# Optimization experiments

Measured on AMD Instinct MI355X. Metric: run time of the kernel, lower is better.

## Reference

```python
import jax, jax.numpy as jnp
import numpy as np

B, C, H, W = 4, 64, 64, 128


def setup_inputs() -> dict:
    key = jax.random.key(0)
    ks = jax.random.split(key, 10)
    s = 1.0 / np.sqrt(C)
    return {
        "query": jax.random.normal(ks[0], (B, C, H, W), dtype=jnp.float32),
        "key_": jax.random.normal(ks[1], (B, C, H, W), dtype=jnp.float32),
        "value": jax.random.normal(ks[2], (B, C, H, W), dtype=jnp.float32),
        "Wq": jax.random.normal(ks[3], (C, C), dtype=jnp.float32) * s,
        "bq": jax.random.normal(ks[4], (C,), dtype=jnp.float32) * s,
        "Wk": jax.random.normal(ks[5], (C, C), dtype=jnp.float32) * s,
        "bk": jax.random.normal(ks[6], (C,), dtype=jnp.float32) * s,
        "Wv": jax.random.normal(ks[7], (C, C), dtype=jnp.float32) * s,
        "bv": jax.random.normal(ks[8], (C,), dtype=jnp.float32) * s,
        "gamma": jax.random.normal(ks[9], (), dtype=jnp.float32) * 0.1,
    }


def reference(query, key_, value, Wq, bq, Wk, bk, Wv, bv, gamma):
    b, c, h, w = query.shape
    n = h * w
    fq = query.reshape(b, c, n)
    fk = key_.reshape(b, c, n)
    fv = value.reshape(b, c, n)
    # 1x1 Conv1d == per-position channel matmul: [C_out, C_in] x [B, C_in, N]
    q = jnp.einsum('oc,bcn->bon', Wq, fq) + bq[:, None]
    k = jnp.einsum('oc,bcn->bon', Wk, fk) + bk[:, None]
    v = jnp.einsum('oc,bcn->bon', Wv, fv) + bv[:, None]
    # query permuted to [B, N, C], bmm with key [B, C, N] -> [B, Nq, Nk]; scale by W (last dim of input shape)
    qk = jnp.einsum('bcn,bcm->bnm', q, k) / w
    # non-standard softmax over dim=1 (query-position axis)
    attn = jax.nn.softmax(qk, axis=1)
    # value [B, C, N] @ attn [B, Nq, Nk] -> [B, C, Nk]
    av = jnp.einsum('bcn,bnm->bcm', v, attn)
    out = gamma * av.reshape(b, c, h, w) + v.reshape(b, c, h, w)
    return out
```

## Files before the change

### kernel.cpp

```cpp
#include <hip/hip_runtime.h>

#define NPOS 8192
#define NC 64
#define NB 4
#define NSPLIT 4
#define NCHUNK 2048
#define QSCALE 0.01127105500167846f

typedef __bf16 bf16x8 __attribute__((ext_vector_type(8)));
typedef __bf16 bf16x4 __attribute__((ext_vector_type(4)));
typedef float f32x4 __attribute__((ext_vector_type(4)));

#define EXP2F(x) __builtin_amdgcn_exp2f(x)

static __device__ __forceinline__ unsigned f2bf_u(float x) {
  unsigned u = __float_as_uint(x);
  return (u + 0x7FFFu + ((u >> 16) & 1u)) >> 16;
}
static __device__ __forceinline__ unsigned pack2(float a, float b) {
  return f2bf_u(a) | (f2bf_u(b) << 16);
}

static __device__ __forceinline__ void gload_lds16(const void* gsrc, void* lds_base) {
  __builtin_amdgcn_global_load_lds(
      (const __attribute__((address_space(1))) unsigned int*)gsrc,
      (__attribute__((address_space(3))) unsigned int*)lds_base, 16, 0, 0);
}

__global__ __launch_bounds__(256) void proj_kernel(
    const float* __restrict__ xq, const float* __restrict__ xk, const float* __restrict__ xv,
    const float* __restrict__ Wq, const float* __restrict__ bq,
    const float* __restrict__ Wk, const float* __restrict__ bk,
    const float* __restrict__ Wv, const float* __restrict__ bv,
    unsigned short* __restrict__ qT, unsigned short* __restrict__ kT,
    unsigned short* __restrict__ vb, float* __restrict__ vf)
{
  __shared__ float sW[NC * NC];
  __shared__ float sB[NC];
  const int p = blockIdx.z, b = blockIdx.y;
  const int n0 = blockIdx.x * 128;
  const int tid = threadIdx.x;
  const int wv = tid >> 6, l = tid & 63;

  const float* x    = p == 0 ? xq : (p == 1 ? xk : xv);
  const float* W    = p == 0 ? Wq : (p == 1 ? Wk : Wv);
  const float* bias = p == 0 ? bq : (p == 1 ? bk : bv);

  for (int i = tid; i < NC * NC; i += 256) sW[i] = W[i];
  if (tid < NC) sB[tid] = bias[tid];
  __syncthreads();

  const int nb = n0 + 2 * l;
  const float* xb = x + (size_t)b * NC * NPOS + nb;

  float acc[16][2];
#pragma unroll
  for (int oi = 0; oi < 16; ++oi) {
    float bz = sB[16 * wv + oi];
    acc[oi][0] = bz; acc[oi][1] = bz;
  }
  for (int c = 0; c < NC; ++c) {
    const float2 x2 = *(const float2*)(xb + (size_t)c * NPOS);
#pragma unroll
    for (int oi = 0; oi < 16; ++oi) {
      float wgt = sW[(16 * wv + oi) * NC + c];
      acc[oi][0] = fmaf(wgt, x2.x, acc[oi][0]);
      acc[oi][1] = fmaf(wgt, x2.y, acc[oi][1]);
    }
  }

  if (p < 2) {
    const float qs = (p == 0) ? QSCALE : 1.0f;
    unsigned short* dst = (p == 0 ? qT : kT) + (size_t)b * NPOS * NC;
#pragma unroll
    for (int r = 0; r < 2; ++r) {
      uint4 w0, w1;
      w0.x = pack2(qs * acc[0][r],  qs * acc[1][r]);
      w0.y = pack2(qs * acc[2][r],  qs * acc[3][r]);
      w0.z = pack2(qs * acc[4][r],  qs * acc[5][r]);
      w0.w = pack2(qs * acc[6][r],  qs * acc[7][r]);
      w1.x = pack2(qs * acc[8][r],  qs * acc[9][r]);
      w1.y = pack2(qs * acc[10][r], qs * acc[11][r]);
      w1.z = pack2(qs * acc[12][r], qs * acc[13][r]);
      w1.w = pack2(qs * acc[14][r], qs * acc[15][r]);
      unsigned short* rp = dst + (size_t)(nb + r) * NC + 16 * wv;
      *(uint4*)(rp) = w0;
      *(uint4*)(rp + 8) = w1;
    }
  } else {
#pragma unroll
    for (int oi = 0; oi < 16; ++oi) {
      const int o = 16 * wv + oi;
      float2 v2;
      v2.x = acc[oi][0]; v2.y = acc[oi][1];
      *(float2*)(vf + ((size_t)b * NC + o) * NPOS + nb) = v2;
      *(unsigned*)(vb + ((size_t)b * NC + o) * NPOS + nb) = pack2(acc[oi][0], acc[oi][1]);
    }
  }
}

__global__ __launch_bounds__(512, 4) void attn_partial(
    const unsigned short* __restrict__ qT,
    const unsigned short* __restrict__ kT,
    const unsigned short* __restrict__ vb,
    float* __restrict__ pav, float* __restrict__ plsum)
{
  __shared__ unsigned short qs_[2][64 * 64];
  __shared__ unsigned short vs_[2][64 * 64];
  __shared__ unsigned short pT[8][16][68];

  const int b = blockIdx.y, z = blockIdx.z;
  const int m0 = blockIdx.x * 256;
  const int tid = threadIdx.x;
  const int w = tid >> 6, l = tid & 63;
  const int lm = l & 15, g = l >> 4;
  const int mA = m0 + 32 * w + lm;
  const int mB = mA + 16;

  const unsigned short* kbA = kT + (size_t)(b * NPOS + mA) * NC + 8 * g;
  const unsigned short* kbB = kT + (size_t)(b * NPOS + mB) * NC + 8 * g;
  const bf16x8 kb0 = *(const bf16x8*)(kbA);
  const bf16x8 kb1 = *(const bf16x8*)(kbA + 32);
  const bf16x8 kb2 = *(const bf16x8*)(kbB);
  const bf16x8 kb3 = *(const bf16x8*)(kbB + 32);

  const char* qb  = (const char*)(qT + (size_t)b * NPOS * NC);
  const char* vbb = (const char*)(vb + (size_t)b * NC * NPOS);

  const int srow = tid >> 3;
  const int slc  = ((tid & 7) * 16) ^ ((srow & 7) << 4);
  const char* qsrc0 = qb + (size_t)srow * 128 + slc;
  const char* vsrc0 = vbb + (size_t)srow * (NPOS * 2) + slc;
  const int ldsoff = w * 512;

  f32x4 accA[4] = {{0,0,0,0},{0,0,0,0},{0,0,0,0},{0,0,0,0}};
  f32x4 accB[4] = {{0,0,0,0},{0,0,0,0},{0,0,0,0},{0,0,0,0}};
  float lsumA = 0.f, lsumB = 0.f;

  const int nbeg = z * NCHUNK;
  const int iters = NCHUNK >> 6;

  gload_lds16(qsrc0 + (size_t)nbeg * 128, &qs_[0][ldsoff]);
  gload_lds16(vsrc0 + (size_t)nbeg * 2,   &vs_[0][ldsoff]);

  const int swz = (lm & 7) << 4;

  int cur = 0;
  for (int t = 0; t < iters; ++t) {
    const int n0 = nbeg + 64 * t;
    __builtin_amdgcn_s_barrier();
    if (t + 1 < iters) {
      gload_lds16(qsrc0 + (size_t)(n0 + 64) * 128, &qs_[cur ^ 1][ldsoff]);
      gload_lds16(vsrc0 + (size_t)(n0 + 64) * 2,   &vs_[cur ^ 1][ldsoff]);
      asm volatile("s_waitcnt vmcnt(2)" ::: "memory");
    } else {
      asm volatile("s_waitcnt vmcnt(0)" ::: "memory");
    }
    __builtin_amdgcn_s_barrier();
    __builtin_amdgcn_sched_barrier(0);

    const unsigned short* qt = qs_[cur];
    const unsigned short* vt = vs_[cur];

    f32x4 s0[4], s1[4];
    __builtin_amdgcn_s_setprio(1);
#pragma unroll
    for (int sub = 0; sub < 4; ++sub) {
      const int nl = 16 * sub + lm;
      bf16x8 qa0 = *(const bf16x8*)(qt + nl * 64 + (((16 * g) ^ swz) >> 1));
      bf16x8 qa1 = *(const bf16x8*)(qt + nl * 64 + (((64 + 16 * g) ^ swz) >> 1));
      f32x4 za = {0, 0, 0, 0};
      za = __builtin_amdgcn_mfma_f32_16x16x32_bf16(qa0, kb0, za, 0, 0, 0);
      za = __builtin_amdgcn_mfma_f32_16x16x32_bf16(qa1, kb1, za, 0, 0, 0);
      s0[sub] = za;
      f32x4 zb = {0, 0, 0, 0};
      zb = __builtin_amdgcn_mfma_f32_16x16x32_bf16(qa0, kb2, zb, 0, 0, 0);
      zb = __builtin_amdgcn_mfma_f32_16x16x32_bf16(qa1, kb3, zb, 0, 0, 0);
      s1[sub] = zb;
    }
    __builtin_amdgcn_s_setprio(0);

#pragma unroll
    for (int sub = 0; sub < 4; ++sub) {
      float p0 = EXP2F(s0[sub][0]);
      float p1 = EXP2F(s0[sub][1]);
      float p2 = EXP2F(s0[sub][2]);
      float p3 = EXP2F(s0[sub][3]);
      lsumA += (p0 + p1) + (p2 + p3);
      bf16x4 pk;
      pk[0] = (__bf16)p0; pk[1] = (__bf16)p1;
      pk[2] = (__bf16)p2; pk[3] = (__bf16)p3;
      *(bf16x4*)&pT[w][lm][16 * sub + 4 * g] = pk;
    }
    bf16x8 va[2][4];
    __builtin_amdgcn_s_setprio(1);
#pragma unroll
    for (int ks = 0; ks < 2; ++ks) {
      bf16x8 pb = *(const bf16x8*)&pT[w][lm][8 * g + 32 * ks];
#pragma unroll
      for (int cs = 0; cs < 4; ++cs) {
        const int vr = 16 * cs + lm;
        va[ks][cs] = *(const bf16x8*)(vt + vr * 64 + (((16 * g + 64 * ks) ^ swz) >> 1));
        accA[cs] = __builtin_amdgcn_mfma_f32_16x16x32_bf16(va[ks][cs], pb, accA[cs], 0, 0, 0);
      }
    }
    __builtin_amdgcn_s_setprio(0);

#pragma unroll
    for (int sub = 0; sub < 4; ++sub) {
      float p0 = EXP2F(s1[sub][0]);
      float p1 = EXP2F(s1[sub][1]);
      float p2 = EXP2F(s1[sub][2]);
      float p3 = EXP2F(s1[sub][3]);
      lsumB += (p0 + p1) + (p2 + p3);
      bf16x4 pk;
      pk[0] = (__bf16)p0; pk[1] = (__bf16)p1;
      pk[2] = (__bf16)p2; pk[3] = (__bf16)p3;
      *(bf16x4*)&pT[w][lm][16 * sub + 4 * g] = pk;
    }
    __builtin_amdgcn_s_setprio(1);
#pragma unroll
    for (int ks = 0; ks < 2; ++ks) {
      bf16x8 pb = *(const bf16x8*)&pT[w][lm][8 * g + 32 * ks];
#pragma unroll
      for (int cs = 0; cs < 4; ++cs) {
        accB[cs] = __builtin_amdgcn_mfma_f32_16x16x32_bf16(va[ks][cs], pb, accB[cs], 0, 0, 0);
      }
    }
    __builtin_amdgcn_s_setprio(0);
    cur ^= 1;
  }

  lsumA += __shfl_xor(lsumA, 16);
  lsumA += __shfl_xor(lsumA, 32);
  lsumB += __shfl_xor(lsumB, 16);
  lsumB += __shfl_xor(lsumB, 32);
  if (l < 16) {
    plsum[((size_t)(z * NB + b) << 13) + mA] = lsumA;
    plsum[((size_t)(z * NB + b) << 13) + mB] = lsumB;
  }

  float* po = pav + ((size_t)((z * NB + b) * NC) << 13);
#pragma unroll
  for (int cs = 0; cs < 4; ++cs) {
#pragma unroll
    for (int r = 0; r < 4; ++r) {
      const int c = 16 * cs + 4 * g + r;
      po[((size_t)c << 13) + mA] = accA[cs][r];
      po[((size_t)c << 13) + mB] = accB[cs][r];
    }
  }
}

__global__ __launch_bounds__(256) void reduce_kernel(
    const float* __restrict__ pav, const float* __restrict__ plsum,
    const float* __restrict__ vf, const float* __restrict__ gamma_p,
    float* __restrict__ out)
{
  const size_t base = ((size_t)blockIdx.x * 256 + threadIdx.x) * 4;
  const int m = (int)(base & (NPOS - 1));
  const int bc = (int)(base >> 13);
  const int b = bc >> 6;

  float4 s = {0, 0, 0, 0};
  float4 L = {0, 0, 0, 0};
#pragma unroll
  for (int zz = 0; zz < NSPLIT; ++zz) {
    const float4 a = *(const float4*)(pav + (((size_t)(zz * NB * NC + bc)) << 13) + m);
    s.x += a.x; s.y += a.y; s.z += a.z; s.w += a.w;
    const float4 q = *(const float4*)(plsum + (((size_t)(zz * NB + b)) << 13) + m);
    L.x += q.x; L.y += q.y; L.z += q.z; L.w += q.w;
  }
  const float gmv = gamma_p[0];
  const float4 v4 = *(const float4*)(vf + base);
  float4 o;
  o.x = gmv * s.x / L.x + v4.x;
  o.y = gmv * s.y / L.y + v4.y;
  o.z = gmv * s.z / L.z + v4.z;
  o.w = gmv * s.w / L.w + v4.w;
  *(float4*)(out + base) = o;
}

extern "C" void kernel_launch(void* const* d_in, const int* in_sizes, int n_in,
                              void* d_out, int out_size, void* d_ws, size_t ws_size,
                              hipStream_t stream) {
  const float* xq = (const float*)d_in[0];
  const float* xk = (const float*)d_in[1];
  const float* xv = (const float*)d_in[2];
  const float* Wq = (const float*)d_in[3];
  const float* bq = (const float*)d_in[4];
  const float* Wk = (const float*)d_in[5];
  const float* bk = (const float*)d_in[6];
  const float* Wv = (const float*)d_in[7];
  const float* bv = (const float*)d_in[8];
  const float* gm = (const float*)d_in[9];
  float* out = (float*)d_out;

  unsigned short* qT   = (unsigned short*)d_ws;
  unsigned short* kT   = qT + (size_t)NB * NPOS * NC;
  unsigned short* vbuf = kT + (size_t)NB * NPOS * NC;
  float* vf    = (float*)(vbuf + (size_t)NB * NPOS * NC);
  float* pav   = vf + (size_t)NB * NC * NPOS;
  float* plsum = pav + (size_t)NSPLIT * NB * NC * NPOS;

  hipLaunchKernelGGL(proj_kernel, dim3(64, 4, 3), dim3(256), 0, stream,
                     xq, xk, xv, Wq, bq, Wk, bk, Wv, bv, qT, kT, vbuf, vf);
  hipLaunchKernelGGL(attn_partial, dim3(NPOS / 256, NB, NSPLIT), dim3(512), 0, stream,
                     qT, kT, vbuf, pav, plsum);
  hipLaunchKernelGGL(reduce_kernel, dim3(2048), dim3(256), 0, stream,
                     pav, plsum, vf, gm, out);
}
```

Before: 109.2 us.

## Split attention tile across warp pairs along key axis with LDS reduction

Each block now covers 128 query-side columns instead of 256. The 8 warps split into 4 column groups times 2 halves of each 64-row n-chunk. Each warp does half the QK and PV MFMAs per chunk, and the two halves' accumulators and row sums are combined through LDS (reusing the Q/V staging buffers) before one warp group writes out. This doubles the grid, which raises parallelism and lowers per-warp latency per iteration. In exchange, each Q/V tile is loaded twice as often across blocks, and an end-of-kernel LDS reduction plus extra barriers is added. The launch-bounds occupancy hint is also dropped.

Measured after the change: 115.6 us. +5.8%, slower.

```diff
diff --git a/kernel.cpp b/kernel.cpp
--- a/kernel.cpp
+++ b/kernel.cpp
@@ -99,7 +99,7 @@
   }
 }
 
-__global__ __launch_bounds__(512, 4) void attn_partial(
+__global__ __launch_bounds__(512) void attn_partial(
     const unsigned short* __restrict__ qT,
     const unsigned short* __restrict__ kT,
     const unsigned short* __restrict__ vb,
@@ -110,11 +110,12 @@
   __shared__ unsigned short pT[8][16][68];
 
   const int b = blockIdx.y, z = blockIdx.z;
-  const int m0 = blockIdx.x * 256;
+  const int m0 = blockIdx.x * 128;
   const int tid = threadIdx.x;
   const int w = tid >> 6, l = tid & 63;
+  const int mg = w & 3, ng = w >> 2;
   const int lm = l & 15, g = l >> 4;
-  const int mA = m0 + 32 * w + lm;
+  const int mA = m0 + 32 * mg + lm;
   const int mB = mA + 16;
 
   const unsigned short* kbA = kT + (size_t)(b * NPOS + mA) * NC + 8 * g;
@@ -162,92 +163,119 @@
     const unsigned short* qt = qs_[cur];
     const unsigned short* vt = vs_[cur];
 
-    f32x4 s0[4], s1[4];
+    f32x4 s0[2], s1[2];
     __builtin_amdgcn_s_setprio(1);
 #pragma unroll
-    for (int sub = 0; sub < 4; ++sub) {
-      const int nl = 16 * sub + lm;
+    for (int i = 0; i < 2; ++i) {
+      const int nl = 16 * (2 * ng + i) + lm;
       bf16x8 qa0 = *(const bf16x8*)(qt + nl * 64 + (((16 * g) ^ swz) >> 1));
       bf16x8 qa1 = *(const bf16x8*)(qt + nl * 64 + (((64 + 16 * g) ^ swz) >> 1));
       f32x4 za = {0, 0, 0, 0};
       za = __builtin_amdgcn_mfma_f32_16x16x32_bf16(qa0, kb0, za, 0, 0, 0);
       za = __builtin_amdgcn_mfma_f32_16x16x32_bf16(qa1, kb1, za, 0, 0, 0);
-      s0[sub] = za;
+      s0[i] = za;
       f32x4 zb = {0, 0, 0, 0};
       zb = __builtin_amdgcn_mfma_f32_16x16x32_bf16(qa0, kb2, zb, 0, 0, 0);
       zb = __builtin_amdgcn_mfma_f32_16x16x32_bf16(qa1, kb3, zb, 0, 0, 0);
-      s1[sub] = zb;
+      s1[i] = zb;
     }
     __builtin_amdgcn_s_setprio(0);
 
 #pragma unroll
-    for (int sub = 0; sub < 4; ++sub) {
-      float p0 = EXP2F(s0[sub][0]);
-      float p1 = EXP2F(s0[sub][1]);
-      float p2 = EXP2F(s0[sub][2]);
-      float p3 = EXP2F(s0[sub][3]);
+    for (int i = 0; i < 2; ++i) {
+      float p0 = EXP2F(s0[i][0]);
+      float p1 = EXP2F(s0[i][1]);
+      float p2 = EXP2F(s0[i][2]);
+      float p3 = EXP2F(s0[i][3]);
       lsumA += (p0 + p1) + (p2 + p3);
       bf16x4 pk;
       pk[0] = (__bf16)p0; pk[1] = (__bf16)p1;
       pk[2] = (__bf16)p2; pk[3] = (__bf16)p3;
-      *(bf16x4*)&pT[w][lm][16 * sub + 4 * g] = pk;
-    }
-    bf16x8 va[2][4];
-    __builtin_amdgcn_s_setprio(1);
-#pragma unroll
-    for (int ks = 0; ks < 2; ++ks) {
-      bf16x8 pb = *(const bf16x8*)&pT[w][lm][8 * g + 32 * ks];
+      *(bf16x4*)&pT[w][lm][32 * ng + 16 * i + 4 * g] = pk;
+    }
+    bf16x8 va[4];
+    {
+      bf16x8 pb = *(const bf16x8*)&pT[w][lm][8 * g + 32 * ng];
+      __builtin_amdgcn_s_setprio(1);
 #pragma unroll
       for (int cs = 0; cs < 4; ++cs) {
         const int vr = 16 * cs + lm;
-        va[ks][cs] = *(const bf16x8*)(vt + vr * 64 + (((16 * g + 64 * ks) ^ swz) >> 1));
-        accA[cs] = __builtin_amdgcn_mfma_f32_16x16x32_bf16(va[ks][cs], pb, accA[cs], 0, 0, 0);
-      }
-    }
-    __builtin_amdgcn_s_setprio(0);
-
-#pragma unroll
-    for (int sub = 0; sub < 4; ++sub) {
-      float p0 = EXP2F(s1[sub][0]);
-      float p1 = EXP2F(s1[sub][1]);
-      float p2 = EXP2F(s1[sub][2]);
-      float p3 = EXP2F(s1[sub][3]);
+        va[cs] = *(const bf16x8*)(vt + vr * 64 + (((16 * g + 64 * ng) ^ swz) >> 1));
+        accA[cs] = __builtin_amdgcn_mfma_f32_16x16x32_bf16(va[cs], pb, accA[cs], 0, 0, 0);
+      }
+      __builtin_amdgcn_s_setprio(0);
+    }
+
+#pragma unroll
+    for (int i = 0; i < 2; ++i) {
+      float p0 = EXP2F(s1[i][0]);
+      float p1 = EXP2F(s1[i][1]);
+      float p2 = EXP2F(s1[i][2]);
+      float p3 = EXP2F(s1[i][3]);
       lsumB += (p0 + p1) + (p2 + p3);
       bf16x4 pk;
       pk[0] = (__bf16)p0; pk[1] = (__bf16)p1;
       pk[2] = (__bf16)p2; pk[3] = (__bf16)p3;
-      *(bf16x4*)&pT[w][lm][16 * sub + 4 * g] = pk;
-    }
-    __builtin_amdgcn_s_setprio(1);
-#pragma unroll
-    for (int ks = 0; ks < 2; ++ks) {
-      bf16x8 pb = *(const bf16x8*)&pT[w][lm][8 * g + 32 * ks];
+      *(bf16x4*)&pT[w][lm][32 * ng + 16 * i + 4 * g] = pk;
+    }
+    {
+      bf16x8 pb = *(const bf16x8*)&pT[w][lm][8 * g + 32 * ng];
+      __builtin_amdgcn_s_setprio(1);
 #pragma unroll
       for (int cs = 0; cs < 4; ++cs) {
-        accB[cs] = __builtin_amdgcn_mfma_f32_16x16x32_bf16(va[ks][cs], pb, accB[cs], 0, 0, 0);
-      }
-    }
-    __builtin_amdgcn_s_setprio(0);
+        accB[cs] = __builtin_amdgcn_mfma_f32_16x16x32_bf16(va[cs], pb, accB[cs], 0, 0, 0);
+      }
+      __builtin_amdgcn_s_setprio(0);
+    }
     cur ^= 1;
   }
 
-  lsumA += __shfl_xor(lsumA, 16);
-  lsumA += __shfl_xor(lsumA, 32);
-  lsumB += __shfl_xor(lsumB, 16);
-  lsumB += __shfl_xor(lsumB, 32);
-  if (l < 16) {
-    plsum[((size_t)(z * NB + b) << 13) + mA] = lsumA;
-    plsum[((size_t)(z * NB + b) << 13) + mB] = lsumB;
-  }
-
-  float* po = pav + ((size_t)((z * NB + b) * NC) << 13);
-#pragma unroll
-  for (int cs = 0; cs < 4; ++cs) {
-#pragma unroll
-    for (int r = 0; r < 4; ++r) {
-      const int c = 16 * cs + 4 * g + r;
-      po[((size_t)c << 13) + mA] = accA[cs][r];
-      po[((size_t)c << 13) + mB] = accB[cs][r];
+  float* racc = (float*)(&qs_[0][0]);
+  float* rls  = (float*)(&vs_[0][0]);
+  const int slot = mg * 64 + l;
+  __builtin_amdgcn_s_barrier();
+  if (ng == 1) {
+#pragma unroll
+    for (int cs = 0; cs < 4; ++cs) {
+#pragma unroll
+      for (int r = 0; r < 4; ++r) {
+        racc[(cs * 4 + r) * 256 + slot] = accA[cs][r];
+        racc[(16 + cs * 4 + r) * 256 + slot] = accB[cs][r];
+      }
+    }
+    rls[slot] = lsumA;
+    rls[256 + slot] = lsumB;
+  }
+  __builtin_amdgcn_s_barrier();
+  if (ng == 0) {
+#pragma unroll
+    for (int cs = 0; cs < 4; ++cs) {
+#pragma unroll
+      for (int r = 0; r < 4; ++r) {
+        accA[cs][r] += racc[(cs * 4 + r) * 256 + slot];
+        accB[cs][r] += racc[(16 + cs * 4 + r) * 256 + slot];
+      }
+    }
+    lsumA += rls[slot];
+    lsumB += rls[256 + slot];
+
+    lsumA += __shfl_xor(lsumA, 16);
+    lsumA += __shfl_xor(lsumA, 32);
+    lsumB += __shfl_xor(lsumB, 16);
+    lsumB += __shfl_xor(lsumB, 32);
+    if (l < 16) {
+      plsum[((size_t)(z * NB + b) << 13) + mA] = lsumA;
+      plsum[((size_t)(z * NB + b) << 13) + mB] = lsumB;
+    }
+    float* po = pav + ((size_t)((z * NB + b) * NC) << 13);
+#pragma unroll
+    for (int cs = 0; cs < 4; ++cs) {
+#pragma unroll
+      for (int r = 0; r < 4; ++r) {
+        const int c = 16 * cs + 4 * g + r;
+        po[((size_t)c << 13) + mA] = accA[cs][r];
+        po[((size_t)c << 13) + mB] = accB[cs][r];
+      }
     }
   }
 }
@@ -305,7 +333,7 @@
 
   hipLaunchKernelGGL(proj_kernel, dim3(64, 4, 3), dim3(256), 0, stream,
                      xq, xk, xv, Wq, bq, Wk, bk, Wv, bv, qT, kT, vbuf, vf);
-  hipLaunchKernelGGL(attn_partial, dim3(NPOS / 256, NB, NSPLIT), dim3(512), 0, stream,
+  hipLaunchKernelGGL(attn_partial, dim3(NPOS / 128, NB, NSPLIT), dim3(512), 0, stream,
                      qT, kT, vbuf, pav, plsum);
   hipLaunchKernelGGL(reduce_kernel, dim3(2048), dim3(256), 0, stream,
                      pav, plsum, vf, gm, out);
```

## Double stage size to 128 positions per barrier and XOR-swizzle P tile

Applied to the files above, without the earlier changes.

The attention loop now loads 128 query/value positions per pipeline stage instead of 64, so there are half as many barrier pairs and wait points per chunk. The inner compute is split into two 64-position halves over the larger LDS tiles. The padded P-transpose buffer is replaced by an unpadded one with an XOR swizzle to avoid bank conflicts, and the occupancy hint in launch_bounds is dropped. LDS use roughly doubles (about 80KB per block), which lowers the number of resident blocks per CU and may hide latency less well.

Measured after the change: 121.2 us. 11.0% more time.

```diff
diff --git a/kernel.cpp b/kernel.cpp
--- a/kernel.cpp
+++ b/kernel.cpp
@@ -99,15 +99,15 @@
   }
 }
 
-__global__ __launch_bounds__(512, 4) void attn_partial(
+__global__ __launch_bounds__(512) void attn_partial(
     const unsigned short* __restrict__ qT,
     const unsigned short* __restrict__ kT,
     const unsigned short* __restrict__ vb,
     float* __restrict__ pav, float* __restrict__ plsum)
 {
-  __shared__ unsigned short qs_[2][64 * 64];
-  __shared__ unsigned short vs_[2][64 * 64];
-  __shared__ unsigned short pT[8][16][68];
+  __shared__ unsigned short qs_[2][128 * 64];
+  __shared__ unsigned short vs_[2][64 * 128];
+  __shared__ unsigned short pTs[8][16][64];
 
   const int b = blockIdx.y, z = blockIdx.z;
   const int m0 = blockIdx.x * 256;
@@ -127,10 +127,12 @@
   const char* qb  = (const char*)(qT + (size_t)b * NPOS * NC);
   const char* vbb = (const char*)(vb + (size_t)b * NC * NPOS);
 
-  const int srow = tid >> 3;
-  const int slc  = ((tid & 7) * 16) ^ ((srow & 7) << 4);
-  const char* qsrc0 = qb + (size_t)srow * 128 + slc;
-  const char* vsrc0 = vbb + (size_t)srow * (NPOS * 2) + slc;
+  const int qrow = tid >> 3;
+  const int qlc  = ((tid & 7) * 16) ^ ((qrow & 7) << 4);
+  const char* qsrc0 = qb + (size_t)qrow * 128 + qlc;
+  const int vrow = tid >> 4;
+  const int vlc  = ((tid & 15) * 16) ^ ((vrow & 7) << 4);
+  const char* vsrc0 = vbb + (size_t)vrow * (NPOS * 2) + vlc;
   const int ldsoff = w * 512;
 
   f32x4 accA[4] = {{0,0,0,0},{0,0,0,0},{0,0,0,0},{0,0,0,0}};
@@ -138,21 +140,29 @@
   float lsumA = 0.f, lsumB = 0.f;
 
   const int nbeg = z * NCHUNK;
-  const int iters = NCHUNK >> 6;
-
-  gload_lds16(qsrc0 + (size_t)nbeg * 128, &qs_[0][ldsoff]);
-  gload_lds16(vsrc0 + (size_t)nbeg * 2,   &vs_[0][ldsoff]);
+  const int iters = NCHUNK >> 7;
+
+#define STAGE(buf, nn)                                                          \
+  do {                                                                          \
+    gload_lds16(qsrc0 + (size_t)(nn) * 128,        &qs_[buf][ldsoff]);          \
+    gload_lds16(qsrc0 + (size_t)((nn) + 64) * 128, &qs_[buf][4096 + ldsoff]);   \
+    gload_lds16(vsrc0 + (size_t)(nn) * 2,          &vs_[buf][ldsoff]);          \
+    gload_lds16(vsrc0 + (size_t)(nn) * 2 + (size_t)32 * (NPOS * 2),             \
+                &vs_[buf][4096 + ldsoff]);                                      \
+  } while (0)
+
+  STAGE(0, nbeg);
 
   const int swz = (lm & 7) << 4;
+  const int ptk = 8 * (lm & 7);
 
   int cur = 0;
   for (int t = 0; t < iters; ++t) {
-    const int n0 = nbeg + 64 * t;
+    const int n0 = nbeg + 128 * t;
     __builtin_amdgcn_s_barrier();
     if (t + 1 < iters) {
-      gload_lds16(qsrc0 + (size_t)(n0 + 64) * 128, &qs_[cur ^ 1][ldsoff]);
-      gload_lds16(vsrc0 + (size_t)(n0 + 64) * 2,   &vs_[cur ^ 1][ldsoff]);
-      asm volatile("s_waitcnt vmcnt(2)" ::: "memory");
+      STAGE(cur ^ 1, n0 + 128);
+      asm volatile("s_waitcnt vmcnt(4)" ::: "memory");
     } else {
       asm volatile("s_waitcnt vmcnt(0)" ::: "memory");
     }
@@ -162,74 +172,79 @@
     const unsigned short* qt = qs_[cur];
     const unsigned short* vt = vs_[cur];
 
-    f32x4 s0[4], s1[4];
-    __builtin_amdgcn_s_setprio(1);
-#pragma unroll
-    for (int sub = 0; sub < 4; ++sub) {
-      const int nl = 16 * sub + lm;
-      bf16x8 qa0 = *(const bf16x8*)(qt + nl * 64 + (((16 * g) ^ swz) >> 1));
-      bf16x8 qa1 = *(const bf16x8*)(qt + nl * 64 + (((64 + 16 * g) ^ swz) >> 1));
-      f32x4 za = {0, 0, 0, 0};
-      za = __builtin_amdgcn_mfma_f32_16x16x32_bf16(qa0, kb0, za, 0, 0, 0);
-      za = __builtin_amdgcn_mfma_f32_16x16x32_bf16(qa1, kb1, za, 0, 0, 0);
-      s0[sub] = za;
-      f32x4 zb = {0, 0, 0, 0};
-      zb = __builtin_amdgcn_mfma_f32_16x16x32_bf16(qa0, kb2, zb, 0, 0, 0);
-      zb = __builtin_amdgcn_mfma_f32_16x16x32_bf16(qa1, kb3, zb, 0, 0, 0);
-      s1[sub] = zb;
-    }
-    __builtin_amdgcn_s_setprio(0);
-
-#pragma unroll
-    for (int sub = 0; sub < 4; ++sub) {
-      float p0 = EXP2F(s0[sub][0]);
-      float p1 = EXP2F(s0[sub][1]);
-      float p2 = EXP2F(s0[sub][2]);
-      float p3 = EXP2F(s0[sub][3]);
-      lsumA += (p0 + p1) + (p2 + p3);
-      bf16x4 pk;
-      pk[0] = (__bf16)p0; pk[1] = (__bf16)p1;
-      pk[2] = (__bf16)p2; pk[3] = (__bf16)p3;
-      *(bf16x4*)&pT[w][lm][16 * sub + 4 * g] = pk;
-    }
-    bf16x8 va[2][4];
-    __builtin_amdgcn_s_setprio(1);
-#pragma unroll
-    for (int ks = 0; ks < 2; ++ks) {
-      bf16x8 pb = *(const bf16x8*)&pT[w][lm][8 * g + 32 * ks];
-#pragma unroll
-      for (int cs = 0; cs < 4; ++cs) {
-        const int vr = 16 * cs + lm;
-        va[ks][cs] = *(const bf16x8*)(vt + vr * 64 + (((16 * g + 64 * ks) ^ swz) >> 1));
-        accA[cs] = __builtin_amdgcn_mfma_f32_16x16x32_bf16(va[ks][cs], pb, accA[cs], 0, 0, 0);
-      }
-    }
-    __builtin_amdgcn_s_setprio(0);
-
-#pragma unroll
-    for (int sub = 0; sub < 4; ++sub) {
-      float p0 = EXP2F(s1[sub][0]);
-      float p1 = EXP2F(s1[sub][1]);
-      float p2 = EXP2F(s1[sub][2]);
-      float p3 = EXP2F(s1[sub][3]);
-      lsumB += (p0 + p1) + (p2 + p3);
-      bf16x4 pk;
-      pk[0] = (__bf16)p0; pk[1] = (__bf16)p1;
-      pk[2] = (__bf16)p2; pk[3] = (__bf16)p3;
-      *(bf16x4*)&pT[w][lm][16 * sub + 4 * g] = pk;
-    }
-    __builtin_amdgcn_s_setprio(1);
-#pragma unroll
-    for (int ks = 0; ks < 2; ++ks) {
-      bf16x8 pb = *(const bf16x8*)&pT[w][lm][8 * g + 32 * ks];
-#pragma unroll
-      for (int cs = 0; cs < 4; ++cs) {
-        accB[cs] = __builtin_amdgcn_mfma_f32_16x16x32_bf16(va[ks][cs], pb, accB[cs], 0, 0, 0);
-      }
-    }
-    __builtin_amdgcn_s_setprio(0);
+#pragma unroll
+    for (int h = 0; h < 2; ++h) {
+      f32x4 s0[4], s1[4];
+      __builtin_amdgcn_s_setprio(1);
+#pragma unroll
+      for (int sub = 0; sub < 4; ++sub) {
+        const int nl = 64 * h + 16 * sub + lm;
+        bf16x8 qa0 = *(const bf16x8*)(qt + nl * 64 + (((16 * g) ^ swz) >> 1));
+        bf16x8 qa1 = *(const bf16x8*)(qt + nl * 64 + (((64 + 16 * g) ^ swz) >> 1));
+        f32x4 za = {0, 0, 0, 0};
+        za = __builtin_amdgcn_mfma_f32_16x16x32_bf16(qa0, kb0, za, 0, 0, 0);
+        za = __builtin_amdgcn_mfma_f32_16x16x32_bf16(qa1, kb1, za, 0, 0, 0);
+        s0[sub] = za;
+        f32x4 zb = {0, 0, 0, 0};
+        zb = __builtin_amdgcn_mfma_f32_16x16x32_bf16(qa0, kb2, zb, 0, 0, 0);
+        zb = __builtin_amdgcn_mfma_f32_16x16x32_bf16(qa1, kb3, zb, 0, 0, 0);
+        s1[sub] = zb;
+      }
+      __builtin_amdgcn_s_setprio(0);
+
+#pragma unroll
+      for (int sub = 0; sub < 4; ++sub) {
+        float p0 = EXP2F(s0[sub][0]);
+        float p1 = EXP2F(s0[sub][1]);
+        float p2 = EXP2F(s0[sub][2]);
+        float p3 = EXP2F(s0[sub][3]);
+        lsumA += (p0 + p1) + (p2 + p3);
+        bf16x4 pk;
+        pk[0] = (__bf16)p0; pk[1] = (__bf16)p1;
+        pk[2] = (__bf16)p2; pk[3] = (__bf16)p3;
+        *(bf16x4*)&pTs[w][lm][(16 * sub + 4 * g) ^ ptk] = pk;
+      }
+      bf16x8 va[2][4];
+      __builtin_amdgcn_s_setprio(1);
+#pragma unroll
+      for (int ks = 0; ks < 2; ++ks) {
+        bf16x8 pb = *(const bf16x8*)&pTs[w][lm][(8 * g + 32 * ks) ^ ptk];
+#pragma unroll
+        for (int cs = 0; cs < 4; ++cs) {
+          const int vr = 16 * cs + lm;
+          va[ks][cs] = *(const bf16x8*)(vt + vr * 128 +
+                          (((16 * g + 64 * ks + 128 * h) ^ swz) >> 1));
+          accA[cs] = __builtin_amdgcn_mfma_f32_16x16x32_bf16(va[ks][cs], pb, accA[cs], 0, 0, 0);
+        }
+      }
+      __builtin_amdgcn_s_setprio(0);
+
+#pragma unroll
+      for (int sub = 0; sub < 4; ++sub) {
+        float p0 = EXP2F(s1[sub][0]);
+        float p1 = EXP2F(s1[sub][1]);
+        float p2 = EXP2F(s1[sub][2]);
+        float p3 = EXP2F(s1[sub][3]);
+        lsumB += (p0 + p1) + (p2 + p3);
+        bf16x4 pk;
+        pk[0] = (__bf16)p0; pk[1] = (__bf16)p1;
+        pk[2] = (__bf16)p2; pk[3] = (__bf16)p3;
+        *(bf16x4*)&pTs[w][lm][(16 * sub + 4 * g) ^ ptk] = pk;
+      }
+      __builtin_amdgcn_s_setprio(1);
+#pragma unroll
+      for (int ks = 0; ks < 2; ++ks) {
+        bf16x8 pb = *(const bf16x8*)&pTs[w][lm][(8 * g + 32 * ks) ^ ptk];
+#pragma unroll
+        for (int cs = 0; cs < 4; ++cs) {
+          accB[cs] = __builtin_amdgcn_mfma_f32_16x16x32_bf16(va[ks][cs], pb, accB[cs], 0, 0, 0);
+        }
+      }
+      __builtin_amdgcn_s_setprio(0);
+    }
     cur ^= 1;
   }
+#undef STAGE
 
   lsumA += __shfl_xor(lsumA, 16);
   lsumA += __shfl_xor(lsumA, 32);
```
